# Kernel optimization log

Measured on AMD Instinct MI355X. Metric: run time of the kernel, lower is better.

## Reference

```python
import jax, jax.numpy as jnp
import numpy as np

INPUT_SIZE = 1024
HIDDEN_SIZE = 1024
N_LAYERS = 2
OUTPUT_SIZE = 4096
BATCH = 4096


def setup_inputs() -> dict:
    key = jax.random.key(0)
    ks = jax.random.split(key, 12)
    s = 1.0 / np.sqrt(HIDDEN_SIZE)
    u = lambda k, shp: jax.random.uniform(k, shp, jnp.float32, -s, s)
    return {
        "input": jax.random.normal(ks[0], (1, BATCH, INPUT_SIZE), jnp.float32),
        "hidden": jax.random.normal(ks[1], (N_LAYERS, BATCH, HIDDEN_SIZE), jnp.float32),
        # nn.RNN layer 0 params
        "W_ih0": u(ks[2], (HIDDEN_SIZE, INPUT_SIZE)),
        "W_hh0": u(ks[3], (HIDDEN_SIZE, HIDDEN_SIZE)),
        "b_ih0": u(ks[4], (HIDDEN_SIZE,)),
        "b_hh0": u(ks[5], (HIDDEN_SIZE,)),
        # nn.RNN layer 1 params (input is layer-0 hidden)
        "W_ih1": u(ks[6], (HIDDEN_SIZE, HIDDEN_SIZE)),
        "W_hh1": u(ks[7], (HIDDEN_SIZE, HIDDEN_SIZE)),
        "b_ih1": u(ks[8], (HIDDEN_SIZE,)),
        "b_hh1": u(ks[9], (HIDDEN_SIZE,)),
        # i2o Linear(input_size + hidden_size, output_size)
        "W_out": u(ks[10], (OUTPUT_SIZE, INPUT_SIZE + HIDDEN_SIZE)),
        "b_out": u(ks[11], (OUTPUT_SIZE,)),
    }


def reference(input, hidden, W_ih0, W_hh0, b_ih0, b_hh0,
              W_ih1, W_hh1, b_ih1, b_hh1, W_out, b_out):
    x = input[0]  # [B, input_size] (seq_len == 1)
    # nn.RNN single step, tanh nonlinearity, 2 layers
    h0 = jnp.tanh(x @ W_ih0.T + b_ih0 + hidden[0] @ W_hh0.T + b_hh0)   # [B, H]
    h1 = jnp.tanh(h0 @ W_ih1.T + b_ih1 + hidden[1] @ W_hh1.T + b_hh1)  # [B, H]
    new_hidden = jnp.stack([h0, h1], axis=0)  # [n_layers, B, H]
    # combined = cat(input[0], hidden[0]) where hidden is the NEW hidden
    combined = jnp.concatenate([x, h0], axis=1)  # [B, input+hidden]
    logits = combined @ W_out.T + b_out          # [B, output_size]
    out = jax.nn.log_softmax(logits, axis=1)
    return (out, new_hidden)
```

## Files before the change

### kernel.cpp

```cpp
#include <hip/hip_runtime.h>
#include <math.h>


typedef __attribute__((ext_vector_type(8))) short bf16x8;
typedef __attribute__((ext_vector_type(4))) float f32x4;

__device__ __forceinline__ unsigned short f2b_rne(float f) {
    unsigned int x = __float_as_uint(f);
    x += 0x7FFF + ((x >> 16) & 1);
    return (unsigned short)(x >> 16);
}

__device__ __forceinline__ void gload_lds16(const void* g, void* l) {
    __builtin_amdgcn_global_load_lds(
        (const __attribute__((address_space(1))) void*)g,
        (__attribute__((address_space(3))) void*)l,
        16, 0, 0);
}

struct CvtSeg { const float* src; unsigned short* dst; unsigned n8; };
struct CvtArgs { CvtSeg seg[8]; };

__global__ __launch_bounds__(256) void f2b_multi(CvtArgs a)
{
    unsigned i = blockIdx.x * 256u + threadIdx.x;
#pragma unroll
    for (int s = 0; s < 8; ++s) {
        if (i < a.seg[s].n8) {
            const float4* src = (const float4*)a.seg[s].src;
            float4 u = src[2 * (size_t)i];
            float4 v = src[2 * (size_t)i + 1];
            unsigned short t[8] = {
                f2b_rne(u.x), f2b_rne(u.y), f2b_rne(u.z), f2b_rne(u.w),
                f2b_rne(v.x), f2b_rne(v.y), f2b_rne(v.z), f2b_rne(v.w)};
            *(uint4*)(a.seg[s].dst + 8 * (size_t)i) = *(const uint4*)t;
            return;
        }
        i -= a.seg[s].n8;
    }
}

struct GemmP {
    const unsigned short *Aa, *Ab; int lda;
    const unsigned short *Wa, *Wb; int ldw;
    const float *ba, *bb;
    float* C; int ldc;
    unsigned short* Cb; int ldcb;
    int nx, nb, do_tanh;
};

template<int BM, int BN>
__device__ __forceinline__ void gemm2p_body(
    const GemmP& p, int bid0, unsigned short* As, unsigned short* Ws, int tid)
{
    constexpr int FM = BM / 32;
    constexpr int FN = BN / 32;
    int bid = (bid0 & 7) * (p.nb >> 3) + (bid0 >> 3);
    const int row0 = (bid / p.nx) * BM;
    const int col0 = (bid % p.nx) * BN;

    const int wid = tid >> 6, lane = tid & 63;
    const int wr = wid >> 1, wc = wid & 1;
    const int fr = lane & 15, fk = lane >> 4;

    f32x4 acc[FM][FN] = {};

    for (int h = 0; h < 2; ++h) {
        const unsigned short* A = h ? p.Ab : p.Aa;
        const unsigned short* W = h ? p.Wb : p.Wa;
        for (int k0 = 0; k0 < 1024; k0 += 32) {
#pragma unroll
            for (int i = 0; i < BM / 64; ++i) {
                int c = i * 256 + wid * 64 + lane;
                int r = c >> 2, ol = c & 3;
                int os = ol ^ ((r >> 1) & 3);
                gload_lds16(A + (size_t)(row0 + r) * p.lda + k0 + os * 8,
                            As + (i * 256 + wid * 64) * 8);
            }
#pragma unroll
            for (int i = 0; i < BN / 64; ++i) {
                int c = i * 256 + wid * 64 + lane;
                int r = c >> 2, ol = c & 3;
                int os = ol ^ ((r >> 1) & 3);
                gload_lds16(W + (size_t)(col0 + r) * p.ldw + k0 + os * 8,
                            Ws + (i * 256 + wid * 64) * 8);
            }
            __syncthreads();

            bf16x8 af[FM], wf[FN];
#pragma unroll
            for (int m = 0; m < FM; ++m) {
                int r = wr * (BM / 2) + m * 16 + fr;
                af[m] = *(const bf16x8*)&As[r * 32 + ((fk ^ ((r >> 1) & 3)) * 8)];
            }
#pragma unroll
            for (int n = 0; n < FN; ++n) {
                int r = wc * (BN / 2) + n * 16 + fr;
                wf[n] = *(const bf16x8*)&Ws[r * 32 + ((fk ^ ((r >> 1) & 3)) * 8)];
            }
#pragma unroll
            for (int m = 0; m < FM; ++m)
#pragma unroll
                for (int n = 0; n < FN; ++n)
                    acc[m][n] = __builtin_amdgcn_mfma_f32_16x16x32_bf16(
                        af[m], wf[n], acc[m][n], 0, 0, 0);
            __syncthreads();
        }
    }

    const bool dot = p.do_tanh != 0;
#pragma unroll
    for (int n = 0; n < FN; ++n) {
        const int col = col0 + wc * (BN / 2) + n * 16 + fr;
        float b = p.ba[col];
        if (p.bb) b += p.bb[col];
#pragma unroll
        for (int m = 0; m < FM; ++m) {
#pragma unroll
            for (int j = 0; j < 4; ++j) {
                const int r = row0 + wr * (BM / 2) + m * 16 + fk * 4 + j;
                float v = acc[m][n][j] + b;
                if (dot) v = tanhf(v);
                p.C[(size_t)r * p.ldc + col] = v;
                if (p.Cb) p.Cb[(size_t)r * p.ldcb + col] = f2b_rne(v);
            }
        }
    }
}

__global__ __launch_bounds__(256) void gemm1_k(GemmP p)
{
    __shared__ __align__(16) unsigned short As[128 * 32];
    __shared__ __align__(16) unsigned short Ws[64 * 32];
    gemm2p_body<128, 64>(p, blockIdx.x, As, Ws, threadIdx.x);
}

__device__ __forceinline__ void logsoftmax_row(float* __restrict__ p, int tid)
{
    const int lane = tid & 63;
    const int wv = tid >> 6;
    __shared__ float redm[4];
    __shared__ float reds[4];

    float4 v[4];
#pragma unroll
    for (int i = 0; i < 4; ++i) v[i] = ((const float4*)p)[i * 256 + tid];

    float m = v[0].x;
#pragma unroll
    for (int i = 0; i < 4; ++i) {
        m = fmaxf(m, fmaxf(fmaxf(v[i].x, v[i].y), fmaxf(v[i].z, v[i].w)));
    }
#pragma unroll
    for (int off = 32; off; off >>= 1) m = fmaxf(m, __shfl_xor(m, off));
    if (lane == 0) redm[wv] = m;
    __syncthreads();
    m = fmaxf(fmaxf(redm[0], redm[1]), fmaxf(redm[2], redm[3]));

    float s = 0.f;
#pragma unroll
    for (int i = 0; i < 4; ++i) {
        s += expf(v[i].x - m); s += expf(v[i].y - m);
        s += expf(v[i].z - m); s += expf(v[i].w - m);
    }
#pragma unroll
    for (int off = 32; off; off >>= 1) s += __shfl_xor(s, off);
    if (lane == 0) reds[wv] = s;
    __syncthreads();
    s = reds[0] + reds[1] + reds[2] + reds[3];

    const float lse = m + logf(s);
#pragma unroll
    for (int i = 0; i < 4; ++i) {
        float4 o;
        o.x = v[i].x - lse; o.y = v[i].y - lse;
        o.z = v[i].z - lse; o.w = v[i].w - lse;
        ((float4*)p)[i * 256 + tid] = o;
    }
}

__global__ __launch_bounds__(256) void g2sm_k(GemmP p, float* __restrict__ logits)
{
    if (blockIdx.x < 512) {
        __shared__ __align__(16) unsigned short As[128 * 32];
        __shared__ __align__(16) unsigned short Ws[64 * 32];
        gemm2p_body<128, 64>(p, blockIdx.x, As, Ws, threadIdx.x);
    } else {
        logsoftmax_row(logits + (size_t)(blockIdx.x - 512) * 4096, threadIdx.x);
    }
}


__device__ __forceinline__ void stage_half8(
    const unsigned short* __restrict__ src, int ld, int base_rc, int tau, int h,
    unsigned short* lds, int wid, int lane, bool isA)
{
    unsigned short* dst = lds + (tau & 1) * 16384 + h * 8192 + wid * 1024;
    const int k0 = (tau & 15) << 6;
#pragma unroll
    for (int i = 0; i < 2; ++i) {
        int c = wid * 128 + i * 64 + lane;
        int ir = c >> 3, cc = c & 7;
        int grow = isA ? (base_rc + h * 64 + (ir & 63) + ((ir >> 6) << 7))
                       : (base_rc + h * 32 + (ir & 31) + ((ir >> 5) << 6));
        int gk = k0 + (((cc ^ ir) & 7) << 3);
        gload_lds16(src + (size_t)grow * ld + gk, dst + i * 512);
    }
}

__global__ __launch_bounds__(512, 2) void gemm8p(
    const unsigned short* __restrict__ Aa, const unsigned short* __restrict__ Ab,
    const unsigned short* __restrict__ Wa, const unsigned short* __restrict__ Wb,
    int lda, int ldw, const float* __restrict__ bias,
    float* __restrict__ C, int ldc, int nx)
{
    constexpr int NT = 32;
    __shared__ __align__(16) unsigned short smem[65536];
    unsigned short* As = smem;
    unsigned short* Bs = smem + 32768;

    int bid = blockIdx.x;
    bid = (bid & 7) * 32 + (bid >> 3);
    const int row0 = (bid / nx) * 256;
    const int col0 = (bid % nx) * 256;

    const int tid = threadIdx.x;
    const int wid = tid >> 6, lane = tid & 63;
    const int wr = wid >> 2, wc = wid & 3;
    const int fr = lane & 15, fk = lane >> 4;
    const int ch0 = fk ^ (fr & 7);
    const int ch1 = ch0 ^ 4;

#define STA8(tau, h) stage_half8(((tau) < 16 ? Aa : Ab), lda, row0, (tau), (h), As, wid, lane, true)
#define STB8(tau, h) stage_half8(((tau) < 16 ? Wa : Wb), ldw, col0, (tau), (h), Bs, wid, lane, false)

#define LDAF(QM) { const unsigned short* Ap_ = Abase + (QM) * 8192;           \
    _Pragma("unroll") for (int mf = 0; mf < 4; ++mf) {                        \
        int ia = wr * 64 + mf * 16 + fr;                                      \
        af[mf][0] = *(const bf16x8*)&Ap_[ia * 64 + ch0 * 8];                  \
        af[mf][1] = *(const bf16x8*)&Ap_[ia * 64 + ch1 * 8]; } }

#define LDWF(QN, WF) { const unsigned short* Bp_ = Bbase + (QN) * 8192;       \
    _Pragma("unroll") for (int nf = 0; nf < 2; ++nf) {                        \
        int ib = wc * 32 + nf * 16 + fr;                                      \
        WF[nf][0] = *(const bf16x8*)&Bp_[ib * 64 + ch0 * 8];                  \
        WF[nf][1] = *(const bf16x8*)&Bp_[ib * 64 + ch1 * 8]; } }

#define MMQ(QM, QN, WF) {                                                     \
    __builtin_amdgcn_s_setprio(1);                                            \
    _Pragma("unroll") for (int mf = 0; mf < 4; ++mf)                          \
    _Pragma("unroll") for (int nf = 0; nf < 2; ++nf) {                        \
        acc[QM][QN][mf][nf] = __builtin_amdgcn_mfma_f32_16x16x32_bf16(        \
            af[mf][0], WF[nf][0], acc[QM][QN][mf][nf], 0, 0, 0);              \
        acc[QM][QN][mf][nf] = __builtin_amdgcn_mfma_f32_16x16x32_bf16(        \
            af[mf][1], WF[nf][1], acc[QM][QN][mf][nf], 0, 0, 0); }            \
    __builtin_amdgcn_s_setprio(0); }

#define BAR() __builtin_amdgcn_s_barrier()
#define LGKM0() asm volatile("s_waitcnt lgkmcnt(0)" ::: "memory")

    f32x4 acc[2][2][4][2] = {};
    bf16x8 af[4][2], wfA[2][2], wfB[2][2];

    STA8(0, 0); STB8(0, 0); STB8(0, 1); STA8(0, 1);
    asm volatile("s_waitcnt vmcnt(4)" ::: "memory");
    BAR();

    for (int t = 0; t < NT; ++t) {
        const unsigned short* Abase = As + (t & 1) * 16384;
        const unsigned short* Bbase = Bs + (t & 1) * 16384;
        const bool more = (t + 1 < NT);

        LDAF(0); LDWF(0, wfA);
        if (more) STA8(t + 1, 0);
        BAR(); LGKM0();
        MMQ(0, 0, wfA);
        if (more) { asm volatile("s_waitcnt vmcnt(4)" ::: "memory"); }
        else      { asm volatile("s_waitcnt vmcnt(2)" ::: "memory"); }
        BAR();

        LDWF(1, wfB);
        if (more) STB8(t + 1, 0);
        BAR(); LGKM0();
        MMQ(0, 1, wfB);
        if (more) { asm volatile("s_waitcnt vmcnt(4)" ::: "memory"); }
        else      { asm volatile("s_waitcnt vmcnt(0)" ::: "memory"); }
        BAR();

        LDAF(1);
        if (more) STB8(t + 1, 1);
        BAR(); LGKM0();
        MMQ(1, 1, wfB);

        if (more) STA8(t + 1, 1);
        MMQ(1, 0, wfA);
        if (more) asm volatile("s_waitcnt vmcnt(4)" ::: "memory");
        BAR();
    }
#undef MMQ
#undef LDAF
#undef LDWF
#undef STA8
#undef STB8
#undef BAR
#undef LGKM0

    float bv[2][2];
#pragma unroll
    for (int qn = 0; qn < 2; ++qn)
#pragma unroll
        for (int nf = 0; nf < 2; ++nf)
            bv[qn][nf] = bias[col0 + wc * 64 + qn * 32 + nf * 16 + fr];

    float* Ct = (float*)smem;
    __syncthreads();
#pragma unroll
    for (int qm = 0; qm < 2; ++qm) {
        if (qm) __syncthreads();
#pragma unroll
        for (int qn = 0; qn < 2; ++qn)
#pragma unroll
            for (int nf = 0; nf < 2; ++nf) {
                const int col = wc * 64 + qn * 32 + nf * 16 + fr;
#pragma unroll
                for (int mf = 0; mf < 4; ++mf)
#pragma unroll
                    for (int j = 0; j < 4; ++j) {
                        int lr = wr * 64 + mf * 16 + fk * 4 + j;
                        int pc = col ^ (((lr >> 2) & 3) << 4);
                        Ct[lr * 256 + pc] = acc[qm][qn][mf][nf][j] + bv[qn][nf];
                    }
            }
        __syncthreads();
#pragma unroll
        for (int k = 0; k < 16; ++k) {
            int idx = k * 512 + tid;
            int lrow = idx >> 6, c4 = idx & 63;
            int pc4 = (c4 * 4) ^ (((lrow >> 2) & 3) << 4);
            int grow = row0 + qm * 64 + (lrow & 63) + ((lrow >> 6) << 7);
            *(float4*)&C[(size_t)grow * ldc + col0 + c4 * 4] =
                *(const float4*)&Ct[lrow * 256 + pc4];
        }
    }
}

extern "C" void kernel_launch(void* const* d_in, const int* in_sizes, int n_in,
                              void* d_out, int out_size, void* d_ws, size_t ws_size,
                              hipStream_t stream)
{
    (void)in_sizes; (void)n_in; (void)out_size; (void)ws_size;

    const float* input  = (const float*)d_in[0];
    const float* hidden = (const float*)d_in[1];
    const float* b_ih0  = (const float*)d_in[4];
    const float* b_hh0  = (const float*)d_in[5];
    const float* b_ih1  = (const float*)d_in[8];
    const float* b_hh1  = (const float*)d_in[9];
    const float* b_out  = (const float*)d_in[11];

    float* out = (float*)d_out;
    float* h0  = out + (size_t)4096 * 4096;
    float* h1  = h0 + (size_t)4096 * 1024;

    unsigned short* xb    = (unsigned short*)d_ws;
    unsigned short* hidb  = xb    + (size_t)4096 * 1024;
    unsigned short* h0b   = hidb  + (size_t)2 * 4096 * 1024;
    unsigned short* Wih0b = h0b   + (size_t)4096 * 1024;
    unsigned short* Whh0b = Wih0b + (size_t)1024 * 1024;
    unsigned short* Wih1b = Whh0b + (size_t)1024 * 1024;
    unsigned short* Whh1b = Wih1b + (size_t)1024 * 1024;
    unsigned short* Woutb = Whh1b + (size_t)1024 * 1024;
    unsigned short* hid0b = hidb;
    unsigned short* hid1b = hidb + (size_t)4096 * 1024;

    CvtArgs ca;
    ca.seg[0] = { input,                 xb,    524288u };
    ca.seg[1] = { hidden,                hidb, 1048576u };
    ca.seg[2] = { (const float*)d_in[2], Wih0b, 131072u };
    ca.seg[3] = { (const float*)d_in[3], Whh0b, 131072u };
    ca.seg[4] = { (const float*)d_in[6], Wih1b, 131072u };
    ca.seg[5] = { (const float*)d_in[7], Whh1b, 131072u };
    ca.seg[6] = { (const float*)d_in[10],Woutb, 1048576u };
    ca.seg[7] = { nullptr, nullptr, 0u };
    hipLaunchKernelGGL(f2b_multi, dim3(12288), dim3(256), 0, stream, ca);

    GemmP p1;
    p1.Aa = xb;    p1.Ab = hid0b; p1.lda = 1024;
    p1.Wa = Wih0b; p1.Wb = Whh0b; p1.ldw = 1024;
    p1.ba = b_ih0; p1.bb = b_hh0;
    p1.C = h0; p1.ldc = 1024; p1.Cb = h0b; p1.ldcb = 1024;
    p1.nx = 16; p1.nb = 512; p1.do_tanh = 1;
    hipLaunchKernelGGL(gemm1_k, dim3(512), dim3(256), 0, stream, p1);

    hipLaunchKernelGGL(gemm8p, dim3(256), dim3(512), 0, stream,
                       xb, h0b, Woutb, Woutb + 1024, 1024, 2048,
                       b_out, out, 4096, 16);

    GemmP p2;
    p2.Aa = h0b;   p2.Ab = hid1b; p2.lda = 1024;
    p2.Wa = Wih1b; p2.Wb = Whh1b; p2.ldw = 1024;
    p2.ba = b_ih1; p2.bb = b_hh1;
    p2.C = h1; p2.ldc = 1024; p2.Cb = nullptr; p2.ldcb = 0;
    p2.nx = 16; p2.nb = 512; p2.do_tanh = 1;
    hipLaunchKernelGGL(g2sm_k, dim3(4608), dim3(256), 0, stream, p2, out);
}
```

Measured before the change: 172.8 us.

## Overlap layer-1 and output weight conversion with layer-0 GEMM; trim barriers

Splits the fp32-to-bf16 conversion so that only the inputs layer 0 needs are converted up front. The remaining conversions (hidden[1], W_ih1, W_hh1, W_out) run in extra blocks of the layer-0 GEMM launch so they overlap with GEMM work. The pipelined output GEMM's main loop also drops several barrier and lgkmcnt waits, moving the vmcnt wait and barrier to the start of each step. This cuts the serial conversion time and sync overhead, but it risks LDS read/write hazards because the explicit lgkmcnt(0) waits before the MFMAs and some barriers are gone.

```diff
diff --git a/kernel.cpp b/kernel.cpp
--- a/kernel.cpp
+++ b/kernel.cpp
@@ -19,13 +19,12 @@
 }
 
 struct CvtSeg { const float* src; unsigned short* dst; unsigned n8; };
-struct CvtArgs { CvtSeg seg[8]; };
-
-__global__ __launch_bounds__(256) void f2b_multi(CvtArgs a)
-{
-    unsigned i = blockIdx.x * 256u + threadIdx.x;
-#pragma unroll
-    for (int s = 0; s < 8; ++s) {
+struct CvtArgs { CvtSeg seg[4]; };
+
+__device__ __forceinline__ void cvt_do(const CvtArgs& a, unsigned i)
+{
+#pragma unroll
+    for (int s = 0; s < 4; ++s) {
         if (i < a.seg[s].n8) {
             const float4* src = (const float4*)a.seg[s].src;
             float4 u = src[2 * (size_t)i];
@@ -40,6 +39,11 @@
     }
 }
 
+__global__ __launch_bounds__(256) void f2b_multi(CvtArgs a)
+{
+    cvt_do(a, blockIdx.x * 256u + threadIdx.x);
+}
+
 struct GemmP {
     const unsigned short *Aa, *Ab; int lda;
     const unsigned short *Wa, *Wb; int ldw;
@@ -128,11 +132,18 @@
     }
 }
 
-__global__ __launch_bounds__(256) void gemm1_k(GemmP p)
-{
-    __shared__ __align__(16) unsigned short As[128 * 32];
-    __shared__ __align__(16) unsigned short Ws[64 * 32];
-    gemm2p_body<128, 64>(p, blockIdx.x, As, Ws, threadIdx.x);
+__global__ __launch_bounds__(256) void g1cvt_k(GemmP p, CvtArgs ca, unsigned total_n8)
+{
+    if (blockIdx.x < 512) {
+        __shared__ __align__(16) unsigned short As[128 * 32];
+        __shared__ __align__(16) unsigned short Ws[64 * 32];
+        gemm2p_body<128, 64>(p, blockIdx.x, As, Ws, threadIdx.x);
+    } else {
+        unsigned i = (blockIdx.x - 512) * 256u + threadIdx.x;
+        const unsigned stride = 512u * 256u;
+        for (unsigned b = 0; b < total_n8; b += stride)
+            cvt_do(ca, b + i);
+    }
 }
 
 __device__ __forceinline__ void logsoftmax_row(float* __restrict__ p, int tid)
@@ -256,54 +267,44 @@
             af[mf][1], WF[nf][1], acc[QM][QN][mf][nf], 0, 0, 0); }            \
     __builtin_amdgcn_s_setprio(0); }
 
-#define BAR() __builtin_amdgcn_s_barrier()
-#define LGKM0() asm volatile("s_waitcnt lgkmcnt(0)" ::: "memory")
-
     f32x4 acc[2][2][4][2] = {};
     bf16x8 af[4][2], wfA[2][2], wfB[2][2];
 
     STA8(0, 0); STB8(0, 0); STB8(0, 1); STA8(0, 1);
-    asm volatile("s_waitcnt vmcnt(4)" ::: "memory");
-    BAR();
 
     for (int t = 0; t < NT; ++t) {
         const unsigned short* Abase = As + (t & 1) * 16384;
         const unsigned short* Bbase = Bs + (t & 1) * 16384;
         const bool more = (t + 1 < NT);
 
+        asm volatile("s_waitcnt vmcnt(4)" ::: "memory");
+        __builtin_amdgcn_s_barrier();
         LDAF(0); LDWF(0, wfA);
         if (more) STA8(t + 1, 0);
-        BAR(); LGKM0();
         MMQ(0, 0, wfA);
+
         if (more) { asm volatile("s_waitcnt vmcnt(4)" ::: "memory"); }
         else      { asm volatile("s_waitcnt vmcnt(2)" ::: "memory"); }
-        BAR();
-
+        __builtin_amdgcn_s_barrier();
         LDWF(1, wfB);
         if (more) STB8(t + 1, 0);
-        BAR(); LGKM0();
         MMQ(0, 1, wfB);
+
         if (more) { asm volatile("s_waitcnt vmcnt(4)" ::: "memory"); }
         else      { asm volatile("s_waitcnt vmcnt(0)" ::: "memory"); }
-        BAR();
-
+        __builtin_amdgcn_s_barrier();
         LDAF(1);
         if (more) STB8(t + 1, 1);
-        BAR(); LGKM0();
         MMQ(1, 1, wfB);
 
         if (more) STA8(t + 1, 1);
         MMQ(1, 0, wfA);
-        if (more) asm volatile("s_waitcnt vmcnt(4)" ::: "memory");
-        BAR();
     }
 #undef MMQ
 #undef LDAF
 #undef LDWF
 #undef STA8
 #undef STB8
-#undef BAR
-#undef LGKM0
 
     float bv[2][2];
 #pragma unroll
@@ -373,16 +374,12 @@
     unsigned short* hid0b = hidb;
     unsigned short* hid1b = hidb + (size_t)4096 * 1024;
 
-    CvtArgs ca;
-    ca.seg[0] = { input,                 xb,    524288u };
-    ca.seg[1] = { hidden,                hidb, 1048576u };
-    ca.seg[2] = { (const float*)d_in[2], Wih0b, 131072u };
-    ca.seg[3] = { (const float*)d_in[3], Whh0b, 131072u };
-    ca.seg[4] = { (const float*)d_in[6], Wih1b, 131072u };
-    ca.seg[5] = { (const float*)d_in[7], Whh1b, 131072u };
-    ca.seg[6] = { (const float*)d_in[10],Woutb, 1048576u };
-    ca.seg[7] = { nullptr, nullptr, 0u };
-    hipLaunchKernelGGL(f2b_multi, dim3(12288), dim3(256), 0, stream, ca);
+    CvtArgs ca1;
+    ca1.seg[0] = { input,                 xb,    524288u };
+    ca1.seg[1] = { hidden,                hid0b, 524288u };
+    ca1.seg[2] = { (const float*)d_in[2], Wih0b, 131072u };
+    ca1.seg[3] = { (const float*)d_in[3], Whh0b, 131072u };
+    hipLaunchKernelGGL(f2b_multi, dim3(5120), dim3(256), 0, stream, ca1);
 
     GemmP p1;
     p1.Aa = xb;    p1.Ab = hid0b; p1.lda = 1024;
@@ -390,7 +387,13 @@
     p1.ba = b_ih0; p1.bb = b_hh0;
     p1.C = h0; p1.ldc = 1024; p1.Cb = h0b; p1.ldcb = 1024;
     p1.nx = 16; p1.nb = 512; p1.do_tanh = 1;
-    hipLaunchKernelGGL(gemm1_k, dim3(512), dim3(256), 0, stream, p1);
+    CvtArgs ca2;
+    ca2.seg[0] = { hidden + (size_t)4096 * 1024, hid1b, 524288u };
+    ca2.seg[1] = { (const float*)d_in[6],  Wih1b, 131072u };
+    ca2.seg[2] = { (const float*)d_in[7],  Whh1b, 131072u };
+    ca2.seg[3] = { (const float*)d_in[10], Woutb, 1048576u };
+    hipLaunchKernelGGL(g1cvt_k, dim3(1024), dim3(256), 0, stream,
+                       p1, ca2, 1835008u);
 
     hipLaunchKernelGGL(gemm8p, dim3(256), dim3(512), 0, stream,
                        xb, h0b, Woutb, Woutb + 1024, 1024, 2048,
```

Result: slower. 208.1 us (+20.4%).
